# Performance work log

Measured on AMD Instinct MI355X. Metric: run time of the kernel, lower is better.

## Reference

```python
import jax, jax.numpy as jnp
import numpy as np

H = 8          # n_heads
DK = 128       # d_model // h
D = H * DK     # d_model = 1024
B, S = 8, 1024
D_LIST = (32, 64, 96, 128)  # sorted set of hidden//h from config dict


def setup_inputs() -> dict:
    key = jax.random.key(0)
    ks = jax.random.split(key, 13)
    mk = lambda k, shape: jax.random.normal(k, shape, dtype=jnp.float32)
    inp = {
        'query': mk(ks[0], (B, S, D)),
        'key': mk(ks[1], (B, S, D)),
        'value': mk(ks[2], (B, S, D)),
        'config_idx': jax.random.randint(ks[3], (B,), 0, len(D_LIST), dtype=jnp.int32),
        'Wq': mk(ks[4], (D, D)) * 0.02, 'bq': jnp.zeros((D,), jnp.float32),
        'Wk': mk(ks[5], (D, D)) * 0.02, 'bk': jnp.zeros((D,), jnp.float32),
        'Wv': mk(ks[6], (D, D)) * 0.02, 'bv': jnp.zeros((D,), jnp.float32),
        'Wo': mk(ks[7], (D, D)) * 0.02, 'bo': jnp.zeros((D,), jnp.float32),
    }
    return inp


def _mha_arrange(query, key, value, config_idx, Wq, bq, Wk, bk, Wv, bv, Wo, bo):
    Bb, Ss, _ = query.shape
    proj = lambda x, W, b: (x @ W.T + b).reshape(Bb, Ss, H, DK).transpose(0, 2, 1, 3)
    q = proj(query, Wq, bq)   # [B,H,S,DK]
    k = proj(key, Wk, bk)
    v = proj(value, Wv, bv)
    scores = jnp.einsum('bhqd,bhkd->bhqk', q, k) / np.float32(np.sqrt(DK))
    p = jax.nn.softmax(scores, axis=-1)
    ctx = jnp.einsum('bhqk,bhkd->bhqd', p, v).transpose(0, 2, 1, 3)  # [B,S,H,DK]
    # attn_arrange: per-sample width d; pack first d dims of each head densely
    ret = jnp.zeros((Bb, Ss, H * DK), query.dtype)
    for i, d in enumerate(D_LIST):
        packed = ctx[:, :, :, :d].reshape(Bb, Ss, H * d)           # [B,S,H*d]
        packed = jnp.pad(packed, ((0, 0), (0, 0), (0, H * (DK - d))))
        sel = (config_idx == i)[:, None, None]
        ret = ret + jnp.where(sel, packed, jnp.zeros((), query.dtype))
    return ret @ Wo.T + bo


def reference(query, key, value, config_idx, Wq, bq, Wk, bk, Wv, bv, Wo, bo):
    return _mha_arrange(query, key, value, config_idx, Wq, bq, Wk, bk, Wv, bv, Wo, bo)
```

## Files before the change

kernel.cpp:

```cpp
#include <hip/hip_runtime.h>
#include <hip/hip_bf16.h>


typedef __attribute__((ext_vector_type(8))) __bf16 bf16x8;
typedef __attribute__((ext_vector_type(4))) float f32x4;

#define DEV static __device__ __forceinline__

DEV float exp2v(float x) { return __builtin_amdgcn_exp2f(x); }

DEV unsigned short f2bf(float f) {
  union { float f; unsigned int u; } c; c.f = f;
  unsigned int u = c.u + 0x7fffu + ((c.u >> 16) & 1u);
  return (unsigned short)(u >> 16);
}

DEV unsigned cvtpk(float a, float b) {
  unsigned r;
  asm("v_cvt_pk_bf16_f32 %0, %1, %2" : "=v"(r) : "v"(a), "v"(b));
  return r;
}

DEV void gload16(const void* g, void* l) {
  __builtin_amdgcn_global_load_lds((const __attribute__((address_space(1))) void*)g,
                                   (__attribute__((address_space(3))) void*)l, 16, 0, 0);
}

#define LGKM0 asm volatile("s_waitcnt lgkmcnt(0)" ::: "memory")
#define BAR   __builtin_amdgcn_s_barrier()
#define VMC6  asm volatile("s_waitcnt vmcnt(6)" ::: "memory")
#define VMC0  asm volatile("s_waitcnt vmcnt(0)" ::: "memory")

DEV void cv4(const float* __restrict__ s, unsigned short* __restrict__ d, int i) {
  const float4 a = *(const float4*)(s + i);
  ushort4 o;
  o.x = f2bf(a.x); o.y = f2bf(a.y); o.z = f2bf(a.z); o.w = f2bf(a.w);
  *(ushort4*)(d + i) = o;
}

__global__ __launch_bounds__(256) void convert_kernel(
    const float* __restrict__ q, const float* __restrict__ k, const float* __restrict__ v,
    const float* __restrict__ wq, const float* __restrict__ wk,
    const float* __restrict__ wv, const float* __restrict__ wo,
    unsigned short* __restrict__ xq, unsigned short* __restrict__ xk,
    unsigned short* __restrict__ xv, unsigned short* __restrict__ wb)
{
  const int i = (blockIdx.x * 256 + threadIdx.x) * 4;
  cv4(q, xq, i);
  cv4(k, xk, i);
  cv4(v, xv, i);
  if (i < 4 * 1024 * 1024) {
    const int which = i >> 20, off = i & 1048575;
    const float* s = which == 0 ? wq : which == 1 ? wk : which == 2 ? wv : wo;
    cv4(s, wb + (which << 20), off);
  }
}

template<int OUTMODE>
__global__ __launch_bounds__(512, 1) void gemmS(
    const unsigned short* __restrict__ xq, const unsigned short* __restrict__ xk,
    const unsigned short* __restrict__ xv, const unsigned short* __restrict__ wb,
    const float* __restrict__ bq, const float* __restrict__ bk,
    const float* __restrict__ bv,
    unsigned short* __restrict__ Qp, unsigned short* __restrict__ Kp,
    unsigned short* __restrict__ VTp, float* __restrict__ fout)
{
  __shared__ __align__(16) char LDS[147456];
  int z, mt, nt;
  if (OUTMODE == 0) {
    const int swz = (blockIdx.x & 7) * 96 + (blockIdx.x >> 3);
    z = swz >> 8; const int rem = swz & 255; mt = rem >> 3; nt = rem & 7;
  } else {
    const int swz = (blockIdx.x & 7) * 32 + (blockIdx.x >> 3);
    z = 0; mt = swz >> 3; nt = swz & 7;
  }
  const int m0 = mt * 256, n0 = nt * 128;
  const unsigned short* Ag = (OUTMODE == 1) ? xq : (z == 0 ? xq : z == 1 ? xk : xv);
  const unsigned short* Bg = (OUTMODE == 1) ? wb : wb + ((size_t)z << 20);
  const float* bias = (OUTMODE == 1) ? bq : (z == 0 ? bq : z == 1 ? bk : bv);

  const int tid = threadIdx.x, lane = tid & 63, w = tid >> 6;
  const int wm = w >> 1, wn = w & 1;
  const int g = lane >> 4, ln = lane & 15;

  const f32x4 fzero = {0.f, 0.f, 0.f, 0.f};
  f32x4 acc[4][4];
#pragma unroll
  for (int i = 0; i < 4; i++)
#pragma unroll
    for (int j = 0; j < 4; j++) acc[i][j] = fzero;

  bf16x8 bfr[4][2];
  bf16x8 afr[2][2];

  auto SA = [&](int bf, int hf, int k0) {
    const unsigned short* src = Ag + (size_t)(m0 + hf * 128) * 1024 + k0;
    char* base = LDS + bf * 32768 + hf * 16384 + w * 2048;
#pragma unroll
    for (int r2 = 0; r2 < 2; ++r2) {
      const int o = w * 2048 + r2 * 1024 + lane * 16;
      const int rwi = o >> 7, cb = o & 127;
      gload16(src + (size_t)rwi * 1024 + ((cb ^ ((rwi & 7) << 4)) >> 1), base + r2 * 1024);
    }
  };
  auto SB = [&](int bf, int k0) {
    const unsigned short* src = Bg + (size_t)n0 * 1024 + k0;
    char* base = LDS + 98304 + bf * 16384 + w * 2048;
#pragma unroll
    for (int r2 = 0; r2 < 2; ++r2) {
      const int o = w * 2048 + r2 * 1024 + lane * 16;
      const int rwi = o >> 7, cb = o & 127;
      gload16(src + (size_t)rwi * 1024 + ((cb ^ ((rwi & 7) << 4)) >> 1), base + r2 * 1024);
    }
  };
  auto rdA = [&](int bf, int q) {
#pragma unroll
    for (int p = 0; p < 2; ++p) {
      const int row = wm * 64 + (2 * q + p) * 16 + ln;
      const int sw = (row & 7) << 4;
#pragma unroll
      for (int kc = 0; kc < 2; ++kc)
        afr[p][kc] = *(const bf16x8*)(LDS + bf * 32768 + row * 128 + ((kc * 64 + g * 16) ^ sw));
    }
  };
  auto rdB = [&](int bf) {
#pragma unroll
    for (int nf = 0; nf < 4; ++nf) {
      const int row = wn * 64 + nf * 16 + ln;
      const int sw = (row & 7) << 4;
#pragma unroll
      for (int kc = 0; kc < 2; ++kc)
        bfr[nf][kc] = *(const bf16x8*)(LDS + 98304 + bf * 16384 + row * 128 + ((kc * 64 + g * 16) ^ sw));
    }
  };
  auto mm = [&](int q) {
    __builtin_amdgcn_s_setprio(1);
#pragma unroll
    for (int p = 0; p < 2; ++p)
#pragma unroll
      for (int nf = 0; nf < 4; ++nf)
#pragma unroll
        for (int kc = 0; kc < 2; ++kc)
          acc[2 * q + p][nf] =
              __builtin_amdgcn_mfma_f32_16x16x32_bf16(afr[p][kc], bfr[nf][kc],
                                                      acc[2 * q + p][nf], 0, 0, 0);
    __builtin_amdgcn_s_setprio(0);
  };

  SA(0, 0, 0); SA(0, 1, 0); SB(0, 0);
  SA(1, 0, 64); SA(1, 1, 64); SB(1, 64);
  VMC6; BAR;

  int br = 0, bw = 2;
  for (int t = 0; t < 16; ++t) {
    const int kL = (t + 2) << 6;
    rdB(br); rdA(br, 0);
    if (t < 14) { SA(bw, 0, kL); SA(bw, 1, kL); }
    BAR; LGKM0; mm(0); BAR;
    rdA(br, 1);
    if (t < 14) SB(bw, kL);
    BAR; LGKM0; mm(1);
    if (t < 14) { VMC6; } else if (t == 14) { VMC0; }
    BAR;
    br = br == 2 ? 0 : br + 1;
    bw = bw == 2 ? 0 : bw + 1;
  }

  const float QS = 0.12751743f;
#pragma unroll
  for (int mf = 0; mf < 4; ++mf)
#pragma unroll
    for (int nf = 0; nf < 4; ++nf) {
      const int m = m0 + wm * 64 + mf * 16 + g * 4;
      const int n = n0 + wn * 64 + nf * 16 + ln;
      const float bn = bias[n];
      if (OUTMODE == 1) {
#pragma unroll
        for (int r = 0; r < 4; ++r)
          fout[(size_t)(m + r) * 1024 + n] = acc[mf][nf][r] + bn;
      } else if (z == 0) {
#pragma unroll
        for (int r = 0; r < 4; ++r)
          Qp[(size_t)(m + r) * 1024 + n] = f2bf((acc[mf][nf][r] + bn) * QS);
      } else if (z == 1) {
#pragma unroll
        for (int r = 0; r < 4; ++r)
          Kp[(size_t)(m + r) * 1024 + n] = f2bf(acc[mf][nf][r] + bn);
      } else {
        const int b = m >> 10, s0 = m & 1023;
        uint2 pk;
        pk.x = cvtpk(acc[mf][nf][0] + bn, acc[mf][nf][1] + bn);
        pk.y = cvtpk(acc[mf][nf][2] + bn, acc[mf][nf][3] + bn);
        *(uint2*)(VTp + (((size_t)(b * 1024 + n)) << 10) + s0) = pk;
      }
    }
}

__global__ __launch_bounds__(512) void attn_kernel(
    const unsigned short* __restrict__ Qp, const unsigned short* __restrict__ Kp,
    const unsigned short* __restrict__ VT, const int* __restrict__ cfg,
    unsigned short* __restrict__ ret)
{
  __shared__ __align__(16) unsigned short Ks[2][64 * 128];
  __shared__ __align__(16) unsigned short Vs[2][128 * 64];
  __shared__ __align__(16) unsigned short Ps[8 * 16 * 64];
  const int bx = blockIdx.x;
  const int qb = bx >> 6, bh = bx & 63, b = bh >> 3, h = bh & 7;
  const int tid = threadIdx.x, lane = tid & 63, w = tid >> 6;
  const int g = lane >> 4, ln = lane & 15;
  const int q0 = qb * 128;
  const f32x4 fzero = {0.f, 0.f, 0.f, 0.f};

  bf16x8 qf[4];
  {
    const unsigned short* qrow = Qp + ((size_t)(b * 1024 + q0 + w * 16 + ln)) * 1024 + h * 128;
#pragma unroll
    for (int kc = 0; kc < 4; kc++) qf[kc] = *(const bf16x8*)(qrow + kc * 32 + g * 8);
  }
  float m_run = -1e30f, l_run = 0.f;
  f32x4 o_acc[8];
#pragma unroll
  for (int i = 0; i < 8; i++) o_acc[i] = fzero;

  auto stage = [&](int buf, int kv0) {
#pragma unroll
    for (int i = 0; i < 2; ++i) {
      const int o = i * 8192 + tid * 16;
      {
        const int r = o >> 8, cb = o & 255;
        const int cs = cb ^ ((r & 7) << 4);
        gload16(Kp + ((size_t)(b * 1024 + kv0 + r)) * 1024 + h * 128 + (cs >> 1),
                (char*)Ks + buf * 16384 + o);
      }
      {
        const int r = o >> 7, cb = o & 127;
        const int cs = cb ^ ((r & 7) << 4);
        gload16(VT + ((size_t)((b * 8 + h) * 128 + r)) * 1024 + kv0 + (cs >> 1),
                (char*)Vs + buf * 16384 + o);
      }
    }
  };

  stage(0, 0);
  asm volatile("s_waitcnt vmcnt(0)" ::: "memory");
  __syncthreads();

  int cur = 0;
  for (int t = 0; t < 16; ++t) {
    if (t < 15) stage(cur ^ 1, (t + 1) * 64);

    f32x4 sc[4];
    __builtin_amdgcn_s_setprio(1);
#pragma unroll
    for (int nb = 0; nb < 4; ++nb) {
      sc[nb] = fzero;
      const int rr = nb * 16 + ln;
      const int sw = (rr & 7) << 4;
#pragma unroll
      for (int kc = 0; kc < 4; ++kc) {
        const bf16x8 kf = *(const bf16x8*)((const char*)Ks + cur * 16384 + rr * 256 +
                                           (((kc * 32 + g * 8) << 1) ^ sw));
        sc[nb] = __builtin_amdgcn_mfma_f32_16x16x32_bf16(kf, qf[kc], sc[nb], 0, 0, 0);
      }
    }
    __builtin_amdgcn_s_setprio(0);

    float mnb[4];
#pragma unroll
    for (int nb = 0; nb < 4; ++nb)
      mnb[nb] = fmaxf(fmaxf(sc[nb][0], sc[nb][1]), fmaxf(sc[nb][2], sc[nb][3]));
    float pmax = fmaxf(fmaxf(mnb[0], mnb[1]), fmaxf(mnb[2], mnb[3]));
    pmax = fmaxf(pmax, __shfl_xor(pmax, 16));
    pmax = fmaxf(pmax, __shfl_xor(pmax, 32));
    if (__any(pmax > m_run + 11.5f)) {
      const float mnew = fmaxf(m_run, pmax);
      const float alpha = exp2v(m_run - mnew);
      l_run *= alpha;
      m_run = mnew;
      float ar[4];
#pragma unroll
      for (int r = 0; r < 4; ++r)
        ar[r] = __shfl(alpha, (lane & 48) | (((lane >> 4) & 3) << 2) | r);
#pragma unroll
      for (int i = 0; i < 8; i++)
#pragma unroll
        for (int r = 0; r < 4; r++) o_acc[i][r] *= ar[r];
    }
    float sum = 0.f;
    float pvv[16];
#pragma unroll
    for (int nb = 0; nb < 4; ++nb)
#pragma unroll
      for (int r = 0; r < 4; ++r) {
        const float p = exp2v(sc[nb][r] - m_run);
        pvv[nb * 4 + r] = p; sum += p;
      }
    l_run += sum;

    {
      char* pbase = (char*)Ps + w * 2048 + ln * 128;
#pragma unroll
      for (int nb = 0; nb < 4; ++nb) {
        uint2 pk;
        pk.x = cvtpk(pvv[nb * 4 + 0], pvv[nb * 4 + 1]);
        pk.y = cvtpk(pvv[nb * 4 + 2], pvv[nb * 4 + 3]);
        *(uint2*)(pbase + (((16 * nb + 4 * g) << 1) ^ ((ln & 7) << 4))) = pk;
      }
    }
    bf16x8 pf[2];
#pragma unroll
    for (int kc = 0; kc < 2; kc++)
      pf[kc] = *(const bf16x8*)((const char*)Ps + w * 2048 + ln * 128 +
                                (((kc * 32 + g * 8) << 1) ^ ((ln & 7) << 4)));

    __builtin_amdgcn_s_setprio(1);
#pragma unroll
    for (int nb2 = 0; nb2 < 8; ++nb2) {
      const int rr = nb2 * 16 + ln;
      const int sw = (rr & 7) << 4;
#pragma unroll
      for (int kc = 0; kc < 2; ++kc) {
        const bf16x8 vf = *(const bf16x8*)((const char*)Vs + cur * 16384 + rr * 128 +
                                           (((kc * 32 + g * 8) << 1) ^ sw));
        o_acc[nb2] = __builtin_amdgcn_mfma_f32_16x16x32_bf16(pf[kc], vf, o_acc[nb2], 0, 0, 0);
      }
    }
    __builtin_amdgcn_s_setprio(0);

    if (t < 15) {
      asm volatile("s_waitcnt vmcnt(0)" ::: "memory");
      __syncthreads();
    }
    cur ^= 1;
  }

  l_run += __shfl_xor(l_run, 16);
  l_run += __shfl_xor(l_run, 32);
  float rl[4];
#pragma unroll
  for (int r = 0; r < 4; ++r)
    rl[r] = 1.0f / __shfl(l_run, (lane & 48) | (((lane >> 4) & 3) << 2) | r);
  const int d_b = 32 * (cfg[b] + 1);
  const int zw = 128 - d_b;
  const size_t rowbase = (size_t)(b * 1024 + q0 + w * 16 + g * 4);
#pragma unroll
  for (int nb2 = 0; nb2 < 8; ++nb2) {
    const int dk = nb2 * 16 + ln;
    if (dk < d_b) {
#pragma unroll
      for (int r = 0; r < 4; r++)
        ret[(rowbase + r) * 1024 + h * d_b + dk] = f2bf(o_acc[nb2][r] * rl[r]);
    } else {
#pragma unroll
      for (int r = 0; r < 4; r++)
        ret[(rowbase + r) * 1024 + 8 * d_b + h * zw + (dk - d_b)] = 0;
    }
  }
}

extern "C" void kernel_launch(void* const* d_in, const int* in_sizes, int n_in,
                              void* d_out, int out_size, void* d_ws, size_t ws_size,
                              hipStream_t stream)
{
  (void)in_sizes; (void)n_in; (void)out_size; (void)ws_size;
  const float* q   = (const float*)d_in[0];
  const float* k   = (const float*)d_in[1];
  const float* v   = (const float*)d_in[2];
  const int*   cfg = (const int*)d_in[3];
  const float* Wq  = (const float*)d_in[4];  const float* bq = (const float*)d_in[5];
  const float* Wk  = (const float*)d_in[6];  const float* bk = (const float*)d_in[7];
  const float* Wv  = (const float*)d_in[8];  const float* bv = (const float*)d_in[9];
  const float* Wo  = (const float*)d_in[10]; const float* bo = (const float*)d_in[11];

  const size_t X  = 8192ull * 1024ull;
  const size_t WN = 1024ull * 1024ull;
  char* p = (char*)d_ws;
  unsigned short* xq  = (unsigned short*)p; p += X * 2;
  unsigned short* xk  = (unsigned short*)p; p += X * 2;
  unsigned short* xv  = (unsigned short*)p; p += X * 2;
  unsigned short* wb  = (unsigned short*)p; p += 4 * WN * 2;
  unsigned short* Qp  = (unsigned short*)p; p += X * 2;
  unsigned short* Kp  = (unsigned short*)p; p += X * 2;
  unsigned short* VTp = (unsigned short*)p; p += X * 2;
  unsigned short* ret = (unsigned short*)p; p += X * 2;

  convert_kernel<<<dim3(8192), dim3(256), 0, stream>>>(q, k, v, Wq, Wk, Wv, Wo,
                                                       xq, xk, xv, wb);

  gemmS<0><<<dim3(768), dim3(512), 0, stream>>>(xq, xk, xv, wb, bq, bk, bv,
                                                Qp, Kp, VTp, nullptr);

  attn_kernel<<<dim3(512), dim3(512), 0, stream>>>(Qp, Kp, VTp, cfg, ret);

  gemmS<1><<<dim3(256), dim3(512), 0, stream>>>(ret, nullptr, nullptr, wb + 3 * WN,
                                                bo, nullptr, nullptr,
                                                nullptr, nullptr, nullptr,
                                                (float*)d_out);
}
```

Measured before the change: 171.5 us.

## Fuse fp32-to-bf16 activation conversion into QKV GEMM A-tile loads

Removes the separate pass that converted the query, key and value activations to bf16 in a workspace. The QKV GEMM now reads fp32 activations directly into registers, converts them with packed bf16 conversion, and writes them into swizzled LDS with a register double-buffered software pipeline. The weight-only conversion kernel is kept. This avoids writing and re-reading about 48MB of bf16 activations, at the cost of more registers, VALU conversion work inside the GEMM loop, and twice the global read bytes per A tile.

```diff
diff --git a/kernel.cpp b/kernel.cpp
--- a/kernel.cpp
+++ b/kernel.cpp
@@ -28,8 +28,8 @@
 
 #define LGKM0 asm volatile("s_waitcnt lgkmcnt(0)" ::: "memory")
 #define BAR   __builtin_amdgcn_s_barrier()
-#define VMC6  asm volatile("s_waitcnt vmcnt(6)" ::: "memory")
-#define VMC0  asm volatile("s_waitcnt vmcnt(0)" ::: "memory")
+#define SCHED0 __builtin_amdgcn_sched_barrier(0)
+#define VMC(n) asm volatile("s_waitcnt vmcnt(" #n ")" ::: "memory")
 
 DEV void cv4(const float* __restrict__ s, unsigned short* __restrict__ d, int i) {
   const float4 a = *(const float4*)(s + i);
@@ -38,46 +38,33 @@
   *(ushort4*)(d + i) = o;
 }
 
-__global__ __launch_bounds__(256) void convert_kernel(
-    const float* __restrict__ q, const float* __restrict__ k, const float* __restrict__ v,
+__global__ __launch_bounds__(256) void convert_w(
     const float* __restrict__ wq, const float* __restrict__ wk,
     const float* __restrict__ wv, const float* __restrict__ wo,
-    unsigned short* __restrict__ xq, unsigned short* __restrict__ xk,
-    unsigned short* __restrict__ xv, unsigned short* __restrict__ wb)
+    unsigned short* __restrict__ wb)
 {
   const int i = (blockIdx.x * 256 + threadIdx.x) * 4;
-  cv4(q, xq, i);
-  cv4(k, xk, i);
-  cv4(v, xv, i);
-  if (i < 4 * 1024 * 1024) {
-    const int which = i >> 20, off = i & 1048575;
-    const float* s = which == 0 ? wq : which == 1 ? wk : which == 2 ? wv : wo;
-    cv4(s, wb + (which << 20), off);
-  }
-}
-
-template<int OUTMODE>
-__global__ __launch_bounds__(512, 1) void gemmS(
-    const unsigned short* __restrict__ xq, const unsigned short* __restrict__ xk,
-    const unsigned short* __restrict__ xv, const unsigned short* __restrict__ wb,
+  const int which = i >> 20, off = i & 1048575;
+  const float* s = which == 0 ? wq : which == 1 ? wk : which == 2 ? wv : wo;
+  cv4(s, wb + (which << 20), off);
+}
+
+__global__ __launch_bounds__(512, 1) void gemm_qkv(
+    const float* __restrict__ Aq, const float* __restrict__ Ak,
+    const float* __restrict__ Av, const unsigned short* __restrict__ wb,
     const float* __restrict__ bq, const float* __restrict__ bk,
     const float* __restrict__ bv,
     unsigned short* __restrict__ Qp, unsigned short* __restrict__ Kp,
-    unsigned short* __restrict__ VTp, float* __restrict__ fout)
+    unsigned short* __restrict__ VTp)
 {
   __shared__ __align__(16) char LDS[147456];
-  int z, mt, nt;
-  if (OUTMODE == 0) {
-    const int swz = (blockIdx.x & 7) * 96 + (blockIdx.x >> 3);
-    z = swz >> 8; const int rem = swz & 255; mt = rem >> 3; nt = rem & 7;
-  } else {
-    const int swz = (blockIdx.x & 7) * 32 + (blockIdx.x >> 3);
-    z = 0; mt = swz >> 3; nt = swz & 7;
-  }
+  const int swz = (blockIdx.x & 7) * 96 + (blockIdx.x >> 3);
+  const int z = swz >> 8; const int rem = swz & 255;
+  const int mt = rem >> 3, nt = rem & 7;
   const int m0 = mt * 256, n0 = nt * 128;
-  const unsigned short* Ag = (OUTMODE == 1) ? xq : (z == 0 ? xq : z == 1 ? xk : xv);
-  const unsigned short* Bg = (OUTMODE == 1) ? wb : wb + ((size_t)z << 20);
-  const float* bias = (OUTMODE == 1) ? bq : (z == 0 ? bq : z == 1 ? bk : bv);
+  const float* Af = z == 0 ? Aq : z == 1 ? Ak : Av;
+  const unsigned short* Bg = wb + ((size_t)z << 20);
+  const float* bias = z == 0 ? bq : z == 1 ? bk : bv;
 
   const int tid = threadIdx.x, lane = tid & 63, w = tid >> 6;
   const int wm = w >> 1, wn = w & 1;
@@ -90,29 +77,39 @@
 #pragma unroll
     for (int j = 0; j < 4; j++) acc[i][j] = fzero;
 
-  bf16x8 bfr[4][2];
-  bf16x8 afr[2][2];
-
-  auto SA = [&](int bf, int hf, int k0) {
-    const unsigned short* src = Ag + (size_t)(m0 + hf * 128) * 1024 + k0;
-    char* base = LDS + bf * 32768 + hf * 16384 + w * 2048;
+  bf16x8 bfr[4][2], afr[2][2];
+
+  auto SB = [&](int bf, int k0) {
+    char* base = LDS + 98304 + bf * 16384 + w * 2048;
 #pragma unroll
     for (int r2 = 0; r2 < 2; ++r2) {
       const int o = w * 2048 + r2 * 1024 + lane * 16;
-      const int rwi = o >> 7, cb = o & 127;
-      gload16(src + (size_t)rwi * 1024 + ((cb ^ ((rwi & 7) << 4)) >> 1), base + r2 * 1024);
-    }
-  };
-  auto SB = [&](int bf, int k0) {
-    const unsigned short* src = Bg + (size_t)n0 * 1024 + k0;
-    char* base = LDS + 98304 + bf * 16384 + w * 2048;
-#pragma unroll
-    for (int r2 = 0; r2 < 2; ++r2) {
-      const int o = w * 2048 + r2 * 1024 + lane * 16;
-      const int rwi = o >> 7, cb = o & 127;
-      gload16(src + (size_t)rwi * 1024 + ((cb ^ ((rwi & 7) << 4)) >> 1), base + r2 * 1024);
-    }
-  };
+      const int row = o >> 7, cb = o & 127;
+      gload16(Bg + (size_t)(n0 + row) * 1024 + k0 + ((cb ^ ((row & 7) << 4)) >> 1),
+              base + r2 * 1024);
+    }
+  };
+
+  const int arow = tid >> 2;
+  const int acol = (tid & 3) << 4;
+  const int wsw  = (arow & 7) << 4;
+  const int wc0  = ((tid & 3) << 5) ^ wsw;
+  const int wc1  = (((tid & 3) << 5) + 16) ^ wsw;
+
+#define LA4(d0, d1, d2, d3, hf, k0) do { \
+    const float* _s = Af + (size_t)(m0 + (hf) * 128 + arow) * 1024 + (k0) + acol; \
+    d0 = *(const float4*)(_s);      d1 = *(const float4*)(_s + 4); \
+    d2 = *(const float4*)(_s + 8);  d3 = *(const float4*)(_s + 12); } while (0)
+
+#define WA4(buf, hf, s0, s1, s2, s3) do { \
+    char* _d = LDS + (buf) * 32768 + (hf) * 16384 + arow * 128; \
+    uint4 _p0, _p1; \
+    _p0.x = cvtpk(s0.x, s0.y); _p0.y = cvtpk(s0.z, s0.w); \
+    _p0.z = cvtpk(s1.x, s1.y); _p0.w = cvtpk(s1.z, s1.w); \
+    _p1.x = cvtpk(s2.x, s2.y); _p1.y = cvtpk(s2.z, s2.w); \
+    _p1.z = cvtpk(s3.x, s3.y); _p1.w = cvtpk(s3.z, s3.w); \
+    *(uint4*)(_d + wc0) = _p0; *(uint4*)(_d + wc1) = _p1; } while (0)
+
   auto rdA = [&](int bf, int q) {
 #pragma unroll
     for (int p = 0; p < 2; ++p) {
@@ -147,9 +144,157 @@
     __builtin_amdgcn_s_setprio(0);
   };
 
+  float4 a00, a01, a02, a03, a04, a05, a06, a07;
+  float4 a10, a11, a12, a13, a14, a15, a16, a17;
+
+  LA4(a00, a01, a02, a03, 0, 0);  LA4(a04, a05, a06, a07, 1, 0);
+  LA4(a10, a11, a12, a13, 0, 64); LA4(a14, a15, a16, a17, 1, 64);
+  SB(0, 0); SB(1, 64);
+  SCHED0;
+  WA4(0, 0, a00, a01, a02, a03);
+  WA4(0, 1, a04, a05, a06, a07);
+  VMC(2);
+  LGKM0; BAR;
+
+#define TILE(t, L0,L1,L2,L3,L4,L5,L6,L7, W0,W1,W2,W3,W4,W5,W6,W7) \
+  do { \
+    const int _kL = ((t) + 2) << 6; \
+     \
+    rdB(br); rdA(br, 0); \
+    if ((t) < 14) LA4(L0, L1, L2, L3, 0, _kL); \
+    SCHED0; \
+    if ((t) < 15) WA4(bn, 0, W0, W1, W2, W3); \
+    BAR; LGKM0; mm(0); BAR; \
+     \
+    rdA(br, 1); \
+    if ((t) < 14) LA4(L4, L5, L6, L7, 1, _kL); \
+    SCHED0; \
+    if ((t) < 15) WA4(bn, 1, W4, W5, W6, W7); \
+    if ((t) < 14) SB(bw, _kL); \
+    BAR; LGKM0; mm(1); \
+    if ((t) < 14) { VMC(10); } else if ((t) == 14) { VMC(0); } \
+    BAR; \
+    br = br == 2 ? 0 : br + 1; \
+    bn = bn == 2 ? 0 : bn + 1; \
+    bw = bw == 2 ? 0 : bw + 1; \
+  } while (0)
+
+  int br = 0, bn = 1, bw = 2;
+  for (int t2 = 0; t2 < 16; t2 += 2) {
+    TILE(t2,     a00, a01, a02, a03, a04, a05, a06, a07,
+                 a10, a11, a12, a13, a14, a15, a16, a17);
+    TILE(t2 + 1, a10, a11, a12, a13, a14, a15, a16, a17,
+                 a00, a01, a02, a03, a04, a05, a06, a07);
+  }
+#undef TILE
+#undef LA4
+#undef WA4
+
+  const float QS = 0.12751743f;
+#pragma unroll
+  for (int mf = 0; mf < 4; ++mf)
+#pragma unroll
+    for (int nf = 0; nf < 4; ++nf) {
+      const int m = m0 + wm * 64 + mf * 16 + g * 4;
+      const int n = n0 + wn * 64 + nf * 16 + ln;
+      const float bn_ = bias[n];
+      if (z == 0) {
+#pragma unroll
+        for (int r = 0; r < 4; ++r)
+          Qp[(size_t)(m + r) * 1024 + n] = f2bf((acc[mf][nf][r] + bn_) * QS);
+      } else if (z == 1) {
+#pragma unroll
+        for (int r = 0; r < 4; ++r)
+          Kp[(size_t)(m + r) * 1024 + n] = f2bf(acc[mf][nf][r] + bn_);
+      } else {
+        const int b = m >> 10, s0 = m & 1023;
+        uint2 pk;
+        pk.x = cvtpk(acc[mf][nf][0] + bn_, acc[mf][nf][1] + bn_);
+        pk.y = cvtpk(acc[mf][nf][2] + bn_, acc[mf][nf][3] + bn_);
+        *(uint2*)(VTp + (((size_t)(b * 1024 + n)) << 10) + s0) = pk;
+      }
+    }
+}
+
+__global__ __launch_bounds__(512, 1) void gemm_out(
+    const unsigned short* __restrict__ Abf, const unsigned short* __restrict__ Bg,
+    const float* __restrict__ bias, float* __restrict__ fout)
+{
+  __shared__ __align__(16) char LDS[147456];
+  const int swz = (blockIdx.x & 7) * 32 + (blockIdx.x >> 3);
+  const int mt = swz >> 3, nt = swz & 7;
+  const int m0 = mt * 256, n0 = nt * 128;
+
+  const int tid = threadIdx.x, lane = tid & 63, w = tid >> 6;
+  const int wm = w >> 1, wn = w & 1;
+  const int g = lane >> 4, ln = lane & 15;
+
+  const f32x4 fzero = {0.f, 0.f, 0.f, 0.f};
+  f32x4 acc[4][4];
+#pragma unroll
+  for (int i = 0; i < 4; i++)
+#pragma unroll
+    for (int j = 0; j < 4; j++) acc[i][j] = fzero;
+
+  bf16x8 bfr[4][2], afr[2][2];
+
+  auto SA = [&](int bf, int hf, int k0) {
+    const unsigned short* src = Abf + (size_t)(m0 + hf * 128) * 1024 + k0;
+    char* base = LDS + bf * 32768 + hf * 16384 + w * 2048;
+#pragma unroll
+    for (int r2 = 0; r2 < 2; ++r2) {
+      const int o = w * 2048 + r2 * 1024 + lane * 16;
+      const int row = o >> 7, cb = o & 127;
+      gload16(src + (size_t)row * 1024 + ((cb ^ ((row & 7) << 4)) >> 1), base + r2 * 1024);
+    }
+  };
+  auto SB = [&](int bf, int k0) {
+    const unsigned short* src = Bg + (size_t)n0 * 1024 + k0;
+    char* base = LDS + 98304 + bf * 16384 + w * 2048;
+#pragma unroll
+    for (int r2 = 0; r2 < 2; ++r2) {
+      const int o = w * 2048 + r2 * 1024 + lane * 16;
+      const int row = o >> 7, cb = o & 127;
+      gload16(src + (size_t)row * 1024 + ((cb ^ ((row & 7) << 4)) >> 1), base + r2 * 1024);
+    }
+  };
+  auto rdA = [&](int bf, int q) {
+#pragma unroll
+    for (int p = 0; p < 2; ++p) {
+      const int row = wm * 64 + (2 * q + p) * 16 + ln;
+      const int sw = (row & 7) << 4;
+#pragma unroll
+      for (int kc = 0; kc < 2; ++kc)
+        afr[p][kc] = *(const bf16x8*)(LDS + bf * 32768 + row * 128 + ((kc * 64 + g * 16) ^ sw));
+    }
+  };
+  auto rdB = [&](int bf) {
+#pragma unroll
+    for (int nf = 0; nf < 4; ++nf) {
+      const int row = wn * 64 + nf * 16 + ln;
+      const int sw = (row & 7) << 4;
+#pragma unroll
+      for (int kc = 0; kc < 2; ++kc)
+        bfr[nf][kc] = *(const bf16x8*)(LDS + 98304 + bf * 16384 + row * 128 + ((kc * 64 + g * 16) ^ sw));
+    }
+  };
+  auto mm = [&](int q) {
+    __builtin_amdgcn_s_setprio(1);
+#pragma unroll
+    for (int p = 0; p < 2; ++p)
+#pragma unroll
+      for (int nf = 0; nf < 4; ++nf)
+#pragma unroll
+        for (int kc = 0; kc < 2; ++kc)
+          acc[2 * q + p][nf] =
+              __builtin_amdgcn_mfma_f32_16x16x32_bf16(afr[p][kc], bfr[nf][kc],
+                                                      acc[2 * q + p][nf], 0, 0, 0);
+    __builtin_amdgcn_s_setprio(0);
+  };
+
   SA(0, 0, 0); SA(0, 1, 0); SB(0, 0);
   SA(1, 0, 64); SA(1, 1, 64); SB(1, 64);
-  VMC6; BAR;
+  VMC(6); BAR;
 
   int br = 0, bw = 2;
   for (int t = 0; t < 16; ++t) {
@@ -160,39 +305,22 @@
     rdA(br, 1);
     if (t < 14) SB(bw, kL);
     BAR; LGKM0; mm(1);
-    if (t < 14) { VMC6; } else if (t == 14) { VMC0; }
+    if (t < 14) { VMC(6); } else if (t == 14) { VMC(0); }
     BAR;
     br = br == 2 ? 0 : br + 1;
     bw = bw == 2 ? 0 : bw + 1;
   }
 
-  const float QS = 0.12751743f;
 #pragma unroll
   for (int mf = 0; mf < 4; ++mf)
 #pragma unroll
     for (int nf = 0; nf < 4; ++nf) {
       const int m = m0 + wm * 64 + mf * 16 + g * 4;
       const int n = n0 + wn * 64 + nf * 16 + ln;
-      const float bn = bias[n];
-      if (OUTMODE == 1) {
-#pragma unroll
-        for (int r = 0; r < 4; ++r)
-          fout[(size_t)(m + r) * 1024 + n] = acc[mf][nf][r] + bn;
-      } else if (z == 0) {
-#pragma unroll
-        for (int r = 0; r < 4; ++r)
-          Qp[(size_t)(m + r) * 1024 + n] = f2bf((acc[mf][nf][r] + bn) * QS);
-      } else if (z == 1) {
-#pragma unroll
-        for (int r = 0; r < 4; ++r)
-          Kp[(size_t)(m + r) * 1024 + n] = f2bf(acc[mf][nf][r] + bn);
-      } else {
-        const int b = m >> 10, s0 = m & 1023;
-        uint2 pk;
-        pk.x = cvtpk(acc[mf][nf][0] + bn, acc[mf][nf][1] + bn);
-        pk.y = cvtpk(acc[mf][nf][2] + bn, acc[mf][nf][3] + bn);
-        *(uint2*)(VTp + (((size_t)(b * 1024 + n)) << 10) + s0) = pk;
-      }
+      const float bn_ = bias[n];
+#pragma unroll
+      for (int r = 0; r < 4; ++r)
+        fout[(size_t)(m + r) * 1024 + n] = acc[mf][nf][r] + bn_;
     }
 }
 
@@ -375,25 +503,18 @@
   const size_t X  = 8192ull * 1024ull;
   const size_t WN = 1024ull * 1024ull;
   char* p = (char*)d_ws;
-  unsigned short* xq  = (unsigned short*)p; p += X * 2;
-  unsigned short* xk  = (unsigned short*)p; p += X * 2;
-  unsigned short* xv  = (unsigned short*)p; p += X * 2;
   unsigned short* wb  = (unsigned short*)p; p += 4 * WN * 2;
   unsigned short* Qp  = (unsigned short*)p; p += X * 2;
   unsigned short* Kp  = (unsigned short*)p; p += X * 2;
   unsigned short* VTp = (unsigned short*)p; p += X * 2;
   unsigned short* ret = (unsigned short*)p; p += X * 2;
 
-  convert_kernel<<<dim3(8192), dim3(256), 0, stream>>>(q, k, v, Wq, Wk, Wv, Wo,
-                                                       xq, xk, xv, wb);
-
-  gemmS<0><<<dim3(768), dim3(512), 0, stream>>>(xq, xk, xv, wb, bq, bk, bv,
-                                                Qp, Kp, VTp, nullptr);
+  convert_w<<<dim3(4096), dim3(256), 0, stream>>>(Wq, Wk, Wv, Wo, wb);
+
+  gemm_qkv<<<dim3(768), dim3(512), 0, stream>>>(q, k, v, wb, bq, bk, bv,
+                                                Qp, Kp, VTp);
 
   attn_kernel<<<dim3(512), dim3(512), 0, stream>>>(Qp, Kp, VTp, cfg, ret);
 
-  gemmS<1><<<dim3(256), dim3(512), 0, stream>>>(ret, nullptr, nullptr, wb + 3 * WN,
-                                                bo, nullptr, nullptr,
-                                                nullptr, nullptr, nullptr,
-                                                (float*)d_out);
-}
+  gemm_out<<<dim3(256), dim3(512), 0, stream>>>(ret, wb + 3 * WN, bo, (float*)d_out);
+}
```

Result: slower. 189.3 us (+10.4%).
